# Optimization experiments

Measured on AMD Instinct MI355X. Metric: run time of the kernel, lower is better.

The kernel has to match this reference:

```python
import jax, jax.numpy as jnp
import numpy as np

EPS = 1e-6
SKIP_THR = 0.35     # AdaptiveComputeBlock skip_threshold
ENERGY_THR = 0.95   # AdaptiveRankLinear energy_threshold


def rms_norm(x, w):
    return x * jax.lax.rsqrt(jnp.mean(x * x, axis=-1, keepdims=True) + EPS) * w


def ternary_quantize(w):
    # absmean quantization: round(w/scale) clamped to {-1,0,+1}, rescaled
    s = jnp.maximum(jnp.mean(jnp.abs(w)), 1e-8)
    return jnp.clip(jnp.round(w / s), -1.0, 1.0) * s


def setup_inputs() -> dict:
    key = jax.random.key(0)
    ks = jax.random.split(key, 16)
    D, H, depth, R, N = 2048, 8192, 2, 16, 4096
    inp = {
        "x": jax.random.normal(ks[0], (N, D), jnp.float32),
        "acb_norm_w": jnp.ones((depth, D), jnp.float32),
        "router_w": jax.random.normal(ks[1], (depth, D), jnp.float32) * 0.02,
        "w1": jax.random.normal(ks[2], (depth, H, D), jnp.float32) * 0.02,
        "w2": jax.random.normal(ks[3], (depth, D, H), jnp.float32) * 0.02,
        "w3": jax.random.normal(ks[4], (depth, H, D), jnp.float32) * 0.02,
        "acb_gamma": jax.random.uniform(ks[5], (depth, D), jnp.float32) * 1e-2,
        "arl_norm_w": jnp.ones((depth, D), jnp.float32),
        "U": jax.random.normal(ks[6], (depth, D, R), jnp.float32) * 0.02,
        "S": jax.random.normal(ks[7], (depth, R), jnp.float32),
        "V": jax.random.normal(ks[8], (depth, R, D), jnp.float32) * 0.02,
        "arl_gamma": jax.random.uniform(ks[9], (depth, D), jnp.float32) * 1e-2,
        "bit_norm_w": jnp.ones((depth, D), jnp.float32),
        "w_up": jax.random.normal(ks[10], (depth, H, D), jnp.float32) * 0.02,
        "w_down": jax.random.normal(ks[11], (depth, D, H), jnp.float32) * 0.02,
        "bit_gamma": jax.random.uniform(ks[12], (depth, D), jnp.float32) * 1e-2,
    }
    return inp


def reference(x, acb_norm_w, router_w, w1, w2, w3, acb_gamma,
              arl_norm_w, U, S, V, arl_gamma,
              bit_norm_w, w_up, w_down, bit_gamma):
    depth = acb_norm_w.shape[0]
    for d in range(depth):
        # ---- AdaptiveComputeBlock (eval path: hard router mask, no gate scaling)
        xn = rms_norm(x, acb_norm_w[d])                    # [N, D]
        gates = jax.nn.sigmoid(xn @ router_w[d])           # [N]
        active = (gates > SKIP_THR)[..., None]             # [N, 1]
        h = jax.nn.silu(xn @ w1[d].T) * (xn @ w3[d].T)     # [N, H] SwiGLU
        ffn = h @ w2[d].T                                  # [N, D]
        x = x + jnp.where(active, ffn * acb_gamma[d], 0.0)

        # ---- AdaptiveRankLinear (effective-rank mask from singular energy)
        xn = rms_norm(x, arl_norm_w[d])
        s_abs = jnp.abs(S[d])
        cum = jnp.cumsum(s_abs) / jnp.maximum(jnp.sum(s_abs), 1e-8)
        # index i kept iff i < r, r = first index with cum >= threshold (plus 1)
        keep = jnp.concatenate([jnp.ones((1,), bool), cum[:-1] < ENERGY_THR])
        low = (xn @ U[d]) * (S[d] * keep)                  # [N, R]
        x = x + (low @ V[d]) * arl_gamma[d]

        # ---- BitLinear (eval path: ternary weights, fp activations)
        xn = rms_norm(x, bit_norm_w[d])
        hq = jax.nn.silu(xn @ ternary_quantize(w_up[d]).T)  # [N, H]
        x = x + (hq @ ternary_quantize(w_down[d]).T) * bit_gamma[d]
    return x
```

## Files before the change

### kernel.cpp

```cpp
#include <hip/hip_runtime.h>

#define D_DIM 2048
#define H_DIM 8192
#define NTOK  4096
#define R_DIM 16
#define DEPTH 2

typedef float f32x4 __attribute__((ext_vector_type(4)));
typedef __bf16 bf16x8 __attribute__((ext_vector_type(8)));
typedef unsigned short u16x4 __attribute__((ext_vector_type(4)));
typedef unsigned short u16x8 __attribute__((ext_vector_type(8)));
typedef int i32x4 __attribute__((ext_vector_type(4)));
typedef int i32x2 __attribute__((ext_vector_type(2)));

typedef __attribute__((address_space(1))) void void_g;
typedef __attribute__((address_space(3))) void void_l;

__device__ __forceinline__ unsigned short f2bf(float f){
  __bf16 b = (__bf16)f;
  return __builtin_bit_cast(unsigned short, b);
}
__device__ __forceinline__ float bf2f(unsigned short u){
  unsigned int x = ((unsigned int)u) << 16;
  return __builtin_bit_cast(float, x);
}

__device__ __forceinline__ float wredf(float v){
#pragma unroll
  for(int o=32;o;o>>=1) v += __shfl_xor(v,o,64);
  return v;
}
__device__ __forceinline__ float wredmax(float v){
#pragma unroll
  for(int o=32;o;o>>=1) v = fmaxf(v, __shfl_xor(v,o,64));
  return v;
}
__device__ __forceinline__ double wredd(double v){
#pragma unroll
  for(int o=32;o;o>>=1) v += __shfl_xor(v,o,64);
  return v;
}

__device__ __forceinline__ void gload_lds16(const void* g, void* l){
  __builtin_amdgcn_global_load_lds((void_g*)g, (void_l*)l, 16, 0, 0);
}

__device__ __forceinline__ int clampi(int v, int lim){
  return v > lim ? lim : (v < -lim ? -lim : v);
}
__device__ __forceinline__ int pack4q(float a, float b, float c, float d,
                                      float inv, int lim){
  int qa = clampi((int)rintf(a*inv), lim);
  int qb = clampi((int)rintf(b*inv), lim);
  int qc = clampi((int)rintf(c*inv), lim);
  int qd = clampi((int)rintf(d*inv), lim);
  return (qa&255) | ((qb&255)<<8) | ((qc&255)<<16) | ((qd&255)<<24);
}

__global__ __launch_bounds__(256) void rowpass1_i8(
    const float* __restrict__ x, const float* __restrict__ nw,
    const float* __restrict__ rw, signed char* __restrict__ xq,
    float* __restrict__ sxn, float* __restrict__ act)
{
  const int row = blockIdx.x, tid = threadIdx.x;
  const int lane = tid & 63, wid = tid >> 6;
  const float* xr = x + (size_t)row*D_DIM + tid*8;
  f32x4 v0 = *(const f32x4*)xr;
  f32x4 v1 = *(const f32x4*)(xr+4);
  float ssq = 0.0f;
#pragma unroll
  for(int j=0;j<4;++j) ssq += v0[j]*v0[j] + v1[j]*v1[j];
  __shared__ float red[4];
  float t = wredf(ssq);
  if(lane==0) red[wid] = t;
  __syncthreads();
  const float rs = rsqrtf((red[0]+red[1]+red[2]+red[3])*(1.0f/D_DIM) + 1e-6f);

  f32x4 n0 = *(const f32x4*)(nw + tid*8);
  f32x4 n1 = *(const f32x4*)(nw + tid*8 + 4);
  f32x4 r0 = *(const f32x4*)(rw + tid*8);
  f32x4 r1 = *(const f32x4*)(rw + tid*8 + 4);
  float a[8];
  float gp = 0.0f, am = 0.0f;
#pragma unroll
  for(int j=0;j<4;++j){
    a[j]   = v0[j]*rs*n0[j];
    a[4+j] = v1[j]*rs*n1[j];
    gp += a[j]*r0[j] + a[4+j]*r1[j];
    am = fmaxf(am, fmaxf(fabsf(a[j]), fabsf(a[4+j])));
  }
  float wm = wredmax(am);
  __syncthreads();
  if(lane==0) red[wid] = wm;
  __syncthreads();
  const float rowmax = fmaxf(fmaxf(red[0],red[1]), fmaxf(red[2],red[3]));
  const float guard = fmaxf(rowmax, 1e-12f);
  const float inv = 127.0f/guard;
  i32x2 q;
  q[0] = pack4q(a[0],a[1],a[2],a[3], inv, 127);
  q[1] = pack4q(a[4],a[5],a[6],a[7], inv, 127);
  *(i32x2*)(xq + (size_t)row*D_DIM + tid*8) = q;

  float gd = wredf(gp);
  __syncthreads();
  if(lane==0) red[wid] = gd;
  __syncthreads();
  if(tid==0){
    sxn[row] = guard/127.0f;
    float dot = red[0]+red[1]+red[2]+red[3];
    float g = 1.0f/(1.0f+expf(-dot));
    act[row] = (g > 0.35f) ? 1.0f : 0.0f;
  }
}

__global__ __launch_bounds__(256) void rowpass2_i8(
    float* __restrict__ x, const float* __restrict__ anw,
    const float* __restrict__ U, const float* __restrict__ Sv,
    const float* __restrict__ V, const float* __restrict__ agam,
    const float* __restrict__ bnw, signed char* __restrict__ xq,
    float* __restrict__ sxn)
{
  const int row = blockIdx.x, tid = threadIdx.x;
  const int lane = tid & 63, wid = tid >> 6;
  float* xr = x + (size_t)row*D_DIM + tid*8;
  f32x4 v0 = *(const f32x4*)xr;
  f32x4 v1 = *(const f32x4*)(xr+4);
  float ssq = 0.0f;
#pragma unroll
  for(int j=0;j<4;++j) ssq += v0[j]*v0[j] + v1[j]*v1[j];
  __shared__ float red[4];
  float t = wredf(ssq);
  if(lane==0) red[wid] = t;
  __syncthreads();
  const float rs = rsqrtf((red[0]+red[1]+red[2]+red[3])*(1.0f/D_DIM) + 1e-6f);

  f32x4 a0 = *(const f32x4*)(anw + tid*8);
  f32x4 a1 = *(const f32x4*)(anw + tid*8 + 4);
  float xn2[8];
#pragma unroll
  for(int j=0;j<4;++j){ xn2[j] = v0[j]*rs*a0[j]; xn2[4+j] = v1[j]*rs*a1[j]; }

  float pl[16];
#pragma unroll
  for(int r2=0;r2<16;++r2) pl[r2] = 0.0f;
#pragma unroll
  for(int j=0;j<8;++j){
    const int k = tid*8 + j;
    const f32x4* Up = (const f32x4*)(U + (size_t)k*R_DIM);
    f32x4 u0=Up[0], u1=Up[1], u2=Up[2], u3=Up[3];
    const float xv = xn2[j];
#pragma unroll
    for(int q=0;q<4;++q){
      pl[q]    += xv*u0[q];
      pl[4+q]  += xv*u1[q];
      pl[8+q]  += xv*u2[q];
      pl[12+q] += xv*u3[q];
    }
  }
#pragma unroll
  for(int r2=0;r2<16;++r2) pl[r2] = wredf(pl[r2]);
  __shared__ float lred[4][16];
  if(lane==0){
#pragma unroll
    for(int r2=0;r2<16;++r2) lred[wid][r2] = pl[r2];
  }
  __syncthreads();
  __shared__ float lowS[16];
  if(tid==0){
    float sa[16]; float totS = 0.0f;
#pragma unroll
    for(int r2=0;r2<16;++r2){ sa[r2] = fabsf(Sv[r2]); totS += sa[r2]; }
    totS = fmaxf(totS, 1e-8f);
    float c = 0.0f;
#pragma unroll
    for(int r2=0;r2<16;++r2){
      float lraw = lred[0][r2]+lred[1][r2]+lred[2][r2]+lred[3][r2];
      float keep = (r2==0) ? 1.0f : ((c/totS < 0.95f) ? 1.0f : 0.0f);
      c += sa[r2];
      lowS[r2] = lraw * Sv[r2] * keep;
    }
  }
  __syncthreads();

  f32x4 d0 = {0,0,0,0}, d1 = {0,0,0,0};
#pragma unroll
  for(int r2=0;r2<16;++r2){
    const float lr = lowS[r2];
    const f32x4* Vp = (const f32x4*)(V + (size_t)r2*D_DIM + tid*8);
    f32x4 q0 = Vp[0], q1 = Vp[1];
#pragma unroll
    for(int j=0;j<4;++j){ d0[j] += lr*q0[j]; d1[j] += lr*q1[j]; }
  }
  f32x4 g0 = *(const f32x4*)(agam + tid*8);
  f32x4 g1 = *(const f32x4*)(agam + tid*8 + 4);
  f32x4 xo0, xo1;
  float ssq2 = 0.0f;
#pragma unroll
  for(int j=0;j<4;++j){
    xo0[j] = v0[j] + d0[j]*g0[j];
    xo1[j] = v1[j] + d1[j]*g1[j];
    ssq2 += xo0[j]*xo0[j] + xo1[j]*xo1[j];
  }
  __syncthreads();
  float t2 = wredf(ssq2);
  if(lane==0) red[wid] = t2;
  __syncthreads();
  const float rs2 = rsqrtf((red[0]+red[1]+red[2]+red[3])*(1.0f/D_DIM) + 1e-6f);
  f32x4 b0 = *(const f32x4*)(bnw + tid*8);
  f32x4 b1 = *(const f32x4*)(bnw + tid*8 + 4);
  float a[8]; float am = 0.0f;
#pragma unroll
  for(int j=0;j<4;++j){
    a[j]   = xo0[j]*rs2*b0[j];
    a[4+j] = xo1[j]*rs2*b1[j];
    am = fmaxf(am, fmaxf(fabsf(a[j]), fabsf(a[4+j])));
  }
  *(f32x4*)xr = xo0;
  *(f32x4*)(xr+4) = xo1;

  float wm = wredmax(am);
  __syncthreads();
  if(lane==0) red[wid] = wm;
  __syncthreads();
  const float rowmax = fmaxf(fmaxf(red[0],red[1]), fmaxf(red[2],red[3]));
  const float guard = fmaxf(rowmax, 1e-12f);
  const float inv = 127.0f/guard;
  i32x2 q;
  q[0] = pack4q(a[0],a[1],a[2],a[3], inv, 127);
  q[1] = pack4q(a[4],a[5],a[6],a[7], inv, 127);
  *(i32x2*)(xq + (size_t)row*D_DIM + tid*8) = q;
  if(tid==0) sxn[row] = guard/127.0f;
}

__global__ __launch_bounds__(256) void hquant(
    const unsigned short* __restrict__ h, signed char* __restrict__ q,
    float* __restrict__ sh)
{
  const int row = blockIdx.x, tid = threadIdx.x;
  const int lane = tid & 63, wid = tid >> 6;
  const unsigned short* hr = h + (size_t)row*H_DIM + tid*32;
  float v[32]; float am = 0.0f;
#pragma unroll
  for(int c=0;c<4;++c){
    u16x8 u = *(const u16x8*)(hr + c*8);
#pragma unroll
    for(int j=0;j<8;++j){
      float f = bf2f(u[j]);
      v[c*8+j] = f;
      am = fmaxf(am, fabsf(f));
    }
  }
  __shared__ float red[4];
  float wm = wredmax(am);
  if(lane==0) red[wid] = wm;
  __syncthreads();
  const float rowmax = fmaxf(fmaxf(red[0],red[1]), fmaxf(red[2],red[3]));
  const float guard = fmaxf(rowmax, 1e-12f);
  const float inv = 127.0f/guard;
  i32x4 o0, o1;
#pragma unroll
  for(int c=0;c<4;++c){
    int p = pack4q(v[c*4],v[c*4+1],v[c*4+2],v[c*4+3], inv, 127);
    o0[c] = p;
  }
#pragma unroll
  for(int c=0;c<4;++c){
    int p = pack4q(v[16+c*4],v[16+c*4+1],v[16+c*4+2],v[16+c*4+3], inv, 127);
    o1[c] = p;
  }
  signed char* qp = q + (size_t)row*H_DIM + tid*32;
  *(i32x4*)qp = o0;
  *(i32x4*)(qp+16) = o1;
  if(tid==0) sh[row] = guard/127.0f;
}

__global__ __launch_bounds__(256) void wmax_part(const float* __restrict__ w,
                                                 float* __restrict__ part)
{
  const long long n4 = (long long)H_DIM*D_DIM/4;
  const int tid = threadIdx.x;
  const int lane = tid & 63, wid = tid >> 6;
  float m = 0.0f;
  for(long long i = (long long)blockIdx.x*256 + tid; i < n4;
      i += (long long)gridDim.x*256){
    f32x4 v = ((const f32x4*)w)[i];
    m = fmaxf(m, fmaxf(fmaxf(fabsf(v[0]),fabsf(v[1])),
                       fmaxf(fabsf(v[2]),fabsf(v[3]))));
  }
  float wm = wredmax(m);
  __shared__ float red[4];
  if(lane==0) red[wid] = wm;
  __syncthreads();
  if(tid==0) part[blockIdx.x] = fmaxf(fmaxf(red[0],red[1]),
                                      fmaxf(red[2],red[3]));
}

__global__ __launch_bounds__(256) void wmax_final(const float* __restrict__ part,
                                                  float* __restrict__ scale)
{
  const int tid = threadIdx.x;
  const int lane = tid & 63, wid = tid >> 6;
  float m = 0.0f;
  for(int i=tid;i<1024;i+=256) m = fmaxf(m, part[i]);
  m = wredmax(m);
  __shared__ float red[4];
  if(lane==0) red[wid] = m;
  __syncthreads();
  if(tid==0){
    float mm = fmaxf(fmaxf(red[0],red[1]), fmaxf(red[2],red[3]));
    scale[0] = fmaxf(mm, 1e-12f)/127.0f;
  }
}

__global__ __launch_bounds__(256) void wquant_i8(const float* __restrict__ w,
                                                 const float* __restrict__ scale,
                                                 signed char* __restrict__ q)
{
  const long long n8 = (long long)H_DIM*D_DIM/8;
  const float inv = 1.0f/scale[0];
  for(long long i = (long long)blockIdx.x*256 + threadIdx.x; i < n8;
      i += (long long)gridDim.x*256){
    f32x4 a = ((const f32x4*)w)[2*i];
    f32x4 b = ((const f32x4*)w)[2*i+1];
    i32x2 o;
    o[0] = pack4q(a[0],a[1],a[2],a[3], inv, 127);
    o[1] = pack4q(b[0],b[1],b[2],b[3], inv, 127);
    ((i32x2*)q)[i] = o;
  }
}

__global__ __launch_bounds__(256) void abs_part(const float* __restrict__ w,
                                                double* __restrict__ part)
{
  const long long n4 = (long long)H_DIM*D_DIM/4;
  const int tid = threadIdx.x;
  const int lane = tid & 63, wid = tid >> 6;
  float s = 0.0f;
  for(long long i = (long long)blockIdx.x*256 + tid; i < n4;
      i += (long long)gridDim.x*256){
    f32x4 v = ((const f32x4*)w)[i];
    s += fabsf(v[0]) + fabsf(v[1]) + fabsf(v[2]) + fabsf(v[3]);
  }
  double ds = wredd((double)s);
  __shared__ double sred[4];
  if(lane==0) sred[wid] = ds;
  __syncthreads();
  if(tid==0) part[blockIdx.x] = sred[0]+sred[1]+sred[2]+sred[3];
}

__global__ __launch_bounds__(256) void abs_final(const double* __restrict__ part,
                                                 float* __restrict__ scale)
{
  const int tid = threadIdx.x;
  const int lane = tid & 63, wid = tid >> 6;
  double s = 0.0;
  for(int i=tid;i<1024;i+=256) s += part[i];
  s = wredd(s);
  __shared__ double sred[4];
  if(lane==0) sred[wid] = s;
  __syncthreads();
  if(tid==0){
    double m = (sred[0]+sred[1]+sred[2]+sred[3]) / ((double)H_DIM*(double)D_DIM);
    scale[0] = (float)fmax(m, 1e-8);
  }
}

__global__ __launch_bounds__(256) void tquant_i8(const float* __restrict__ w,
                                                 const float* __restrict__ scale,
                                                 signed char* __restrict__ q)
{
  const long long n8 = (long long)H_DIM*D_DIM/8;
  const float inv = 1.0f/scale[0];
  for(long long i = (long long)blockIdx.x*256 + threadIdx.x; i < n8;
      i += (long long)gridDim.x*256){
    f32x4 a = ((const f32x4*)w)[2*i];
    f32x4 b = ((const f32x4*)w)[2*i+1];
    i32x2 o;
    o[0] = pack4q(a[0],a[1],a[2],a[3], inv, 1);
    o[1] = pack4q(b[0],b[1],b[2],b[3], inv, 1);
    ((i32x2*)q)[i] = o;
  }
}

template<int EPI, bool DUAL>
__global__ __launch_bounds__(256, DUAL?2:3) void gemm128q(
    const signed char* __restrict__ A,
    const signed char* __restrict__ B0,
    const signed char* __restrict__ B1,
    const int Nout, const int K,
    const float* __restrict__ sArow,
    const float* __restrict__ sW0p,
    const float* __restrict__ sW1p,
    unsigned short* __restrict__ obf,
    float* __restrict__ xacc,
    const float* __restrict__ gamma,
    const float* __restrict__ act)
{
  __shared__ __align__(16) signed char smA[128*64];
  __shared__ __align__(16) signed char smB[128*64];
  __shared__ __align__(16) signed char smB2[DUAL?(128*64):16];

  const int tid  = threadIdx.x;
  const int lane = tid & 63;
  const int wid  = tid >> 6;
  const int wr   = wid >> 1;
  const int wc   = wid & 1;
  const int frow = lane & 15;
  const int k16  = lane >> 4;

  const int nwg = (int)gridDim.x;
  const int bid = (int)blockIdx.x;
  const int swz = ((bid & 7) * (nwg >> 3)) + (bid >> 3);
  const int rowBase = (swz & 31) << 7;
  const int colBase = (swz >> 5) << 7;

  int srow[2], schk[2];
#pragma unroll
  for(int r=0;r<2;++r){
    int t = tid + (r<<8);
    srow[r] = t >> 2;
    schk[r] = (t & 3) ^ ((srow[r] >> 1) & 3);
  }

  const i32x4 izero = {0,0,0,0};
  i32x4 acc[4][4];
  i32x4 acc2[4][4];
#pragma unroll
  for(int m=0;m<4;++m)
#pragma unroll
    for(int n=0;n<4;++n){ acc[m][n] = izero; acc2[m][n] = izero; }

  for(int k0=0;k0<K;k0+=64){
#pragma unroll
    for(int r=0;r<2;++r){
      const signed char* s = A + (size_t)(rowBase+srow[r])*K + k0 + schk[r]*16;
      gload_lds16(s, &smA[((r<<8)+(wid<<6))*16]);
    }
#pragma unroll
    for(int r=0;r<2;++r){
      const signed char* s = B0 + (size_t)(colBase+srow[r])*K + k0 + schk[r]*16;
      gload_lds16(s, &smB[((r<<8)+(wid<<6))*16]);
    }
    if constexpr (DUAL){
#pragma unroll
      for(int r=0;r<2;++r){
        const signed char* s = B1 + (size_t)(colBase+srow[r])*K + k0 + schk[r]*16;
        gload_lds16(s, &smB2[((r<<8)+(wid<<6))*16]);
      }
    }
    __syncthreads();

    i32x4 af[4];
#pragma unroll
    for(int m=0;m<4;++m){
      int rr = (wr<<6)+(m<<4)+frow;
      int ch = k16 ^ ((rr>>1)&3);
      af[m] = *(const i32x4*)&smA[rr*64 + ch*16];
    }
    i32x4 bfr[4];
    i32x4 bfr2[4];
#pragma unroll
    for(int n=0;n<4;++n){
      int rr = (wc<<6)+(n<<4)+frow;
      int ch = k16 ^ ((rr>>1)&3);
      bfr[n] = *(const i32x4*)&smB[rr*64 + ch*16];
      if constexpr (DUAL) bfr2[n] = *(const i32x4*)&smB2[rr*64 + ch*16];
    }
#pragma unroll
    for(int m=0;m<4;++m)
#pragma unroll
      for(int n=0;n<4;++n){
        acc[m][n] = __builtin_amdgcn_mfma_i32_16x16x64_i8(af[m], bfr[n], acc[m][n], 0,0,0);
        if constexpr (DUAL)
          acc2[m][n] = __builtin_amdgcn_mfma_i32_16x16x64_i8(af[m], bfr2[n], acc2[m][n], 0,0,0);
      }
    __syncthreads();
  }

  const float fsW0 = sW0p[0];
  const float fsW1 = DUAL ? sW1p[0] : 0.0f;
  const int growB = rowBase + (wr<<6) + (k16<<2);
  const int gcolB = colBase + (wc<<6) + frow;
#pragma unroll
  for(int m=0;m<4;++m){
#pragma unroll
    for(int n=0;n<4;++n){
      const int grow0 = growB + (m<<4);
      const int gcol  = gcolB + (n<<4);
      i32x4 v = acc[m][n];
      if constexpr (EPI==0){
        i32x4 v2 = acc2[m][n];
#pragma unroll
        for(int j=0;j<4;++j){
          const float sa = sArow[grow0+j];
          float f1 = (float)v[j]  * sa * fsW0;
          float f3 = (float)v2[j] * sa * fsW1;
          float hv = (f1/(1.0f+expf(-f1))) * f3;
          obf[(size_t)(grow0+j)*Nout + gcol] = f2bf(hv);
        }
      } else if constexpr (EPI==1){
#pragma unroll
        for(int j=0;j<4;++j){
          const float sa = sArow[grow0+j];
          float f = (float)v[j] * sa * fsW0;
          obf[(size_t)(grow0+j)*Nout + gcol] = f2bf(f/(1.0f+expf(-f)));
        }
      } else if constexpr (EPI==2){
        const float g = gamma[gcol];
#pragma unroll
        for(int j=0;j<4;++j){
          if(act[grow0+j] != 0.0f){
            const float sa = sArow[grow0+j];
            const size_t ix = (size_t)(grow0+j)*Nout + gcol;
            xacc[ix] += (float)v[j] * sa * fsW0 * g;
          }
        }
      } else {
        const float g = gamma[gcol];
#pragma unroll
        for(int j=0;j<4;++j){
          const float sa = sArow[grow0+j];
          const size_t ix = (size_t)(grow0+j)*Nout + gcol;
          xacc[ix] += (float)v[j] * sa * fsW0 * g;
        }
      }
    }
  }
}

__global__ __launch_bounds__(256) void rowpass1(
    const float* __restrict__ x, const float* __restrict__ nw,
    const float* __restrict__ rw, unsigned short* __restrict__ xn,
    float* __restrict__ act)
{
  const int row = blockIdx.x, tid = threadIdx.x;
  const int lane = tid & 63, wid = tid >> 6;
  const float* xr = x + (size_t)row*D_DIM + tid*8;
  f32x4 v0 = *(const f32x4*)xr;
  f32x4 v1 = *(const f32x4*)(xr+4);
  float ssq = 0.0f;
#pragma unroll
  for(int j=0;j<4;++j) ssq += v0[j]*v0[j] + v1[j]*v1[j];
  __shared__ float red[4];
  float t = wredf(ssq);
  if(lane==0) red[wid] = t;
  __syncthreads();
  const float rs = rsqrtf((red[0]+red[1]+red[2]+red[3])*(1.0f/D_DIM) + 1e-6f);
  f32x4 n0 = *(const f32x4*)(nw + tid*8);
  f32x4 n1 = *(const f32x4*)(nw + tid*8 + 4);
  f32x4 r0 = *(const f32x4*)(rw + tid*8);
  f32x4 r1 = *(const f32x4*)(rw + tid*8 + 4);
  float gp = 0.0f;
  u16x4 o0, o1;
#pragma unroll
  for(int j=0;j<4;++j){
    float a = v0[j]*rs*n0[j];
    float b = v1[j]*rs*n1[j];
    gp += a*r0[j] + b*r1[j];
    o0[j] = f2bf(a);
    o1[j] = f2bf(b);
  }
  unsigned short* xp = xn + (size_t)row*D_DIM + tid*8;
  *(u16x4*)xp = o0;
  *(u16x4*)(xp+4) = o1;
  float gd = wredf(gp);
  __syncthreads();
  if(lane==0) red[wid] = gd;
  __syncthreads();
  if(tid==0){
    float dot = red[0]+red[1]+red[2]+red[3];
    float g = 1.0f/(1.0f+expf(-dot));
    act[row] = (g > 0.35f) ? 1.0f : 0.0f;
  }
}

__global__ __launch_bounds__(256) void rowpass2(
    float* __restrict__ x, const float* __restrict__ anw,
    const float* __restrict__ U, const float* __restrict__ Sv,
    const float* __restrict__ V, const float* __restrict__ agam,
    const float* __restrict__ bnw, unsigned short* __restrict__ xn3)
{
  const int row = blockIdx.x, tid = threadIdx.x;
  const int lane = tid & 63, wid = tid >> 6;
  float* xr = x + (size_t)row*D_DIM + tid*8;
  f32x4 v0 = *(const f32x4*)xr;
  f32x4 v1 = *(const f32x4*)(xr+4);
  float ssq = 0.0f;
#pragma unroll
  for(int j=0;j<4;++j) ssq += v0[j]*v0[j] + v1[j]*v1[j];
  __shared__ float red[4];
  float t = wredf(ssq);
  if(lane==0) red[wid] = t;
  __syncthreads();
  const float rs = rsqrtf((red[0]+red[1]+red[2]+red[3])*(1.0f/D_DIM) + 1e-6f);
  f32x4 a0 = *(const f32x4*)(anw + tid*8);
  f32x4 a1 = *(const f32x4*)(anw + tid*8 + 4);
  float xn2[8];
#pragma unroll
  for(int j=0;j<4;++j){ xn2[j] = v0[j]*rs*a0[j]; xn2[4+j] = v1[j]*rs*a1[j]; }
  float pl[16];
#pragma unroll
  for(int r2=0;r2<16;++r2) pl[r2] = 0.0f;
#pragma unroll
  for(int j=0;j<8;++j){
    const int k = tid*8 + j;
    const f32x4* Up = (const f32x4*)(U + (size_t)k*R_DIM);
    f32x4 u0=Up[0], u1=Up[1], u2=Up[2], u3=Up[3];
    const float xv = xn2[j];
#pragma unroll
    for(int q=0;q<4;++q){
      pl[q] += xv*u0[q]; pl[4+q] += xv*u1[q];
      pl[8+q] += xv*u2[q]; pl[12+q] += xv*u3[q];
    }
  }
#pragma unroll
  for(int r2=0;r2<16;++r2) pl[r2] = wredf(pl[r2]);
  __shared__ float lred[4][16];
  if(lane==0){
#pragma unroll
    for(int r2=0;r2<16;++r2) lred[wid][r2] = pl[r2];
  }
  __syncthreads();
  __shared__ float lowS[16];
  if(tid==0){
    float sa[16]; float totS = 0.0f;
#pragma unroll
    for(int r2=0;r2<16;++r2){ sa[r2] = fabsf(Sv[r2]); totS += sa[r2]; }
    totS = fmaxf(totS, 1e-8f);
    float c = 0.0f;
#pragma unroll
    for(int r2=0;r2<16;++r2){
      float lraw = lred[0][r2]+lred[1][r2]+lred[2][r2]+lred[3][r2];
      float keep = (r2==0) ? 1.0f : ((c/totS < 0.95f) ? 1.0f : 0.0f);
      c += sa[r2];
      lowS[r2] = lraw * Sv[r2] * keep;
    }
  }
  __syncthreads();
  f32x4 d0 = {0,0,0,0}, d1 = {0,0,0,0};
#pragma unroll
  for(int r2=0;r2<16;++r2){
    const float lr = lowS[r2];
    const f32x4* Vp = (const f32x4*)(V + (size_t)r2*D_DIM + tid*8);
    f32x4 q0 = Vp[0], q1 = Vp[1];
#pragma unroll
    for(int j=0;j<4;++j){ d0[j] += lr*q0[j]; d1[j] += lr*q1[j]; }
  }
  f32x4 g0 = *(const f32x4*)(agam + tid*8);
  f32x4 g1 = *(const f32x4*)(agam + tid*8 + 4);
  f32x4 xo0, xo1;
  float ssq2 = 0.0f;
#pragma unroll
  for(int j=0;j<4;++j){
    xo0[j] = v0[j] + d0[j]*g0[j];
    xo1[j] = v1[j] + d1[j]*g1[j];
    ssq2 += xo0[j]*xo0[j] + xo1[j]*xo1[j];
  }
  __syncthreads();
  float t2 = wredf(ssq2);
  if(lane==0) red[wid] = t2;
  __syncthreads();
  const float rs2 = rsqrtf((red[0]+red[1]+red[2]+red[3])*(1.0f/D_DIM) + 1e-6f);
  f32x4 b0 = *(const f32x4*)(bnw + tid*8);
  f32x4 b1 = *(const f32x4*)(bnw + tid*8 + 4);
  u16x4 o0, o1;
#pragma unroll
  for(int j=0;j<4;++j){
    o0[j] = f2bf(xo0[j]*rs2*b0[j]);
    o1[j] = f2bf(xo1[j]*rs2*b1[j]);
  }
  *(f32x4*)xr = xo0;
  *(f32x4*)(xr+4) = xo1;
  unsigned short* xp = xn3 + (size_t)row*D_DIM + tid*8;
  *(u16x4*)xp = o0;
  *(u16x4*)(xp+4) = o1;
}

__global__ __launch_bounds__(256) void tquant(const float* __restrict__ w,
                                              const float* __restrict__ scale,
                                              unsigned short* __restrict__ q)
{
  const long long n4 = (long long)H_DIM*D_DIM/4;
  const float s = scale[0];
  for(long long i = (long long)blockIdx.x*256 + threadIdx.x; i < n4;
      i += (long long)gridDim.x*256){
    f32x4 v = ((const f32x4*)w)[i];
    u16x4 o;
#pragma unroll
    for(int j=0;j<4;++j){
      float r = rintf(v[j]/s);
      r = fminf(1.0f, fmaxf(-1.0f, r));
      o[j] = f2bf(r*s);
    }
    ((u16x4*)q)[i] = o;
  }
}

template<int EPI, bool BBF16, bool DUAL>
__global__ __launch_bounds__(256, DUAL?2:3) void gemm128(
    const unsigned short* __restrict__ A,
    const void* __restrict__ B0v,
    const void* __restrict__ B1v,
    const int Nout, const int K,
    unsigned short* __restrict__ obf,
    float* __restrict__ xacc,
    const float* __restrict__ gamma,
    const float* __restrict__ act)
{
  __shared__ __align__(16) unsigned short smA[128*32];
  __shared__ __align__(16) unsigned short smB[128*32];
  __shared__ __align__(16) unsigned short smB2[DUAL?(128*32):8];

  const int tid  = threadIdx.x;
  const int lane = tid & 63;
  const int wid  = tid >> 6;
  const int wr   = wid >> 1;
  const int wc   = wid & 1;
  const int frow = lane & 15;
  const int k16  = lane >> 4;

  const int nwg = (int)gridDim.x;
  const int bid = (int)blockIdx.x;
  const int swz = ((bid & 7) * (nwg >> 3)) + (bid >> 3);
  const int rowBase = (swz & 31) << 7;
  const int colBase = (swz >> 5) << 7;

  int srow[2], schk[2];
#pragma unroll
  for(int r=0;r<2;++r){
    int t = tid + (r<<8);
    srow[r] = t >> 2;
    schk[r] = (t & 3) ^ ((srow[r] >> 1) & 3);
  }

  const f32x4 vzero = {0.0f,0.0f,0.0f,0.0f};
  f32x4 acc[4][4];
  f32x4 acc2[4][4];
#pragma unroll
  for(int m=0;m<4;++m)
#pragma unroll
    for(int n=0;n<4;++n){ acc[m][n] = vzero; acc2[m][n] = vzero; }

  for(int k0=0;k0<K;k0+=32){
#pragma unroll
    for(int r=0;r<2;++r){
      const unsigned short* s = A + (size_t)(rowBase+srow[r])*K + k0 + schk[r]*8;
      gload_lds16(s, &smA[((r<<8)+(wid<<6))*8]);
    }
    if constexpr (BBF16){
      const unsigned short* B0 = (const unsigned short*)B0v;
#pragma unroll
      for(int r=0;r<2;++r){
        const unsigned short* s = B0 + (size_t)(colBase+srow[r])*K + k0 + schk[r]*8;
        gload_lds16(s, &smB[((r<<8)+(wid<<6))*8]);
      }
    } else {
      const float* B0 = (const float*)B0v;
#pragma unroll
      for(int r=0;r<2;++r){
        const float* s = B0 + (size_t)(colBase+srow[r])*K + k0 + schk[r]*8;
        f32x4 f0 = *(const f32x4*)s;
        f32x4 f1 = *(const f32x4*)(s+4);
        u16x8 o;
#pragma unroll
        for(int j=0;j<4;++j){ o[j] = f2bf(f0[j]); o[4+j] = f2bf(f1[j]); }
        *(u16x8*)&smB[(size_t)(tid+(r<<8))*8] = o;
      }
      if constexpr (DUAL){
        const float* B1 = (const float*)B1v;
#pragma unroll
        for(int r=0;r<2;++r){
          const float* s = B1 + (size_t)(colBase+srow[r])*K + k0 + schk[r]*8;
          f32x4 f0 = *(const f32x4*)s;
          f32x4 f1 = *(const f32x4*)(s+4);
          u16x8 o;
#pragma unroll
          for(int j=0;j<4;++j){ o[j] = f2bf(f0[j]); o[4+j] = f2bf(f1[j]); }
          *(u16x8*)&smB2[(size_t)(tid+(r<<8))*8] = o;
        }
      }
    }
    __syncthreads();

    bf16x8 af[4];
#pragma unroll
    for(int m=0;m<4;++m){
      int rr = (wr<<6)+(m<<4)+frow;
      int ch = k16 ^ ((rr>>1)&3);
      af[m] = *(const bf16x8*)&smA[rr*32 + ch*8];
    }
    bf16x8 bfr[4];
    bf16x8 bfr2[4];
#pragma unroll
    for(int n=0;n<4;++n){
      int rr = (wc<<6)+(n<<4)+frow;
      int ch = k16 ^ ((rr>>1)&3);
      bfr[n] = *(const bf16x8*)&smB[rr*32 + ch*8];
      if constexpr (DUAL) bfr2[n] = *(const bf16x8*)&smB2[rr*32 + ch*8];
    }
#pragma unroll
    for(int m=0;m<4;++m)
#pragma unroll
      for(int n=0;n<4;++n){
        acc[m][n] = __builtin_amdgcn_mfma_f32_16x16x32_bf16(af[m], bfr[n], acc[m][n], 0,0,0);
        if constexpr (DUAL)
          acc2[m][n] = __builtin_amdgcn_mfma_f32_16x16x32_bf16(af[m], bfr2[n], acc2[m][n], 0,0,0);
      }
    __syncthreads();
  }

  const int growB = rowBase + (wr<<6) + (k16<<2);
  const int gcolB = colBase + (wc<<6) + frow;
#pragma unroll
  for(int m=0;m<4;++m){
#pragma unroll
    for(int n=0;n<4;++n){
      const int grow0 = growB + (m<<4);
      const int gcol  = gcolB + (n<<4);
      f32x4 v = acc[m][n];
      if constexpr (EPI==0){
        f32x4 v2 = acc2[m][n];
#pragma unroll
        for(int j=0;j<4;++j){
          float t1 = v[j];
          float hv = (t1/(1.0f+expf(-t1))) * v2[j];
          obf[(size_t)(grow0+j)*Nout + gcol] = f2bf(hv);
        }
      } else if constexpr (EPI==1){
#pragma unroll
        for(int j=0;j<4;++j){
          float t1 = v[j];
          obf[(size_t)(grow0+j)*Nout + gcol] = f2bf(t1/(1.0f+expf(-t1)));
        }
      } else if constexpr (EPI==2){
        const float g = gamma[gcol];
#pragma unroll
        for(int j=0;j<4;++j){
          if(act[grow0+j] != 0.0f){
            const size_t ix = (size_t)(grow0+j)*Nout + gcol;
            xacc[ix] += v[j]*g;
          }
        }
      } else {
        const float g = gamma[gcol];
#pragma unroll
        for(int j=0;j<4;++j){
          const size_t ix = (size_t)(grow0+j)*Nout + gcol;
          xacc[ix] += v[j]*g;
        }
      }
    }
  }
}

extern "C" void kernel_launch(void* const* d_in, const int* in_sizes, int n_in,
                              void* d_out, int out_size, void* d_ws, size_t ws_size,
                              hipStream_t stream)
{
  (void)in_sizes; (void)n_in; (void)out_size;
  const float* x_in  = (const float*)d_in[0];
  const float* acbnw = (const float*)d_in[1];
  const float* routw = (const float*)d_in[2];
  const float* w1    = (const float*)d_in[3];
  const float* w2    = (const float*)d_in[4];
  const float* w3    = (const float*)d_in[5];
  const float* acbg  = (const float*)d_in[6];
  const float* arlnw = (const float*)d_in[7];
  const float* U     = (const float*)d_in[8];
  const float* Sv    = (const float*)d_in[9];
  const float* V     = (const float*)d_in[10];
  const float* arlg  = (const float*)d_in[11];
  const float* bitnw = (const float*)d_in[12];
  const float* wup   = (const float*)d_in[13];
  const float* wdn   = (const float*)d_in[14];
  const float* bitg  = (const float*)d_in[15];

  float* xs = (float*)d_out;
  char* ws = (char*)d_ws;

  const bool big = (ws_size >= (size_t)185000000);

  hipMemcpyAsync(xs, x_in, (size_t)NTOK*D_DIM*sizeof(float),
                 hipMemcpyDeviceToDevice, stream);

  if (big) {
    const size_t MB = 1048576;
    unsigned short* hb   = (unsigned short*)(ws);
    signed char*    xnq  = (signed char*)(ws + 64*MB);
    signed char*    hbq  = (signed char*)(ws + 72*MB);
    signed char*    slotA= (signed char*)(ws + 104*MB);
    signed char*    slotB= (signed char*)(ws + 120*MB);
    char* tail = ws + 136*MB;
    float*  sxn   = (float*)(tail);
    float*  sh    = (float*)(tail + 16384);
    float*  act   = (float*)(tail + 32768);
    float*  fpart = (float*)(tail + 49152);
    double* dpart = (double*)(tail + 57344);
    float*  scb   = (float*)(tail + 65536);

    const int gH = 2048;
    const int gD = 512;

    for(int d=0; d<DEPTH; ++d){
      const size_t oD  = (size_t)d*D_DIM;
      const size_t oHD = (size_t)d*H_DIM*D_DIM;
      const size_t oR  = (size_t)d*R_DIM;
      const size_t oDR = (size_t)d*D_DIM*R_DIM;

      wmax_part<<<1024,256,0,stream>>>(w1+oHD, fpart);
      wmax_final<<<1,256,0,stream>>>(fpart, scb+0);
      wquant_i8<<<2048,256,0,stream>>>(w1+oHD, scb+0, slotA);
      wmax_part<<<1024,256,0,stream>>>(w3+oHD, fpart);
      wmax_final<<<1,256,0,stream>>>(fpart, scb+1);
      wquant_i8<<<2048,256,0,stream>>>(w3+oHD, scb+1, slotB);
      rowpass1_i8<<<NTOK,256,0,stream>>>(xs, acbnw+oD, routw+oD, xnq, sxn, act);
      gemm128q<0,true><<<gH,256,0,stream>>>(
          xnq, slotA, slotB, H_DIM, D_DIM, sxn, scb+0, scb+1,
          hb, nullptr, nullptr, nullptr);
      wmax_part<<<1024,256,0,stream>>>(w2+oHD, fpart);
      wmax_final<<<1,256,0,stream>>>(fpart, scb+2);
      wquant_i8<<<2048,256,0,stream>>>(w2+oHD, scb+2, slotA);
      hquant<<<NTOK,256,0,stream>>>(hb, hbq, sh);
      gemm128q<2,false><<<gD,256,0,stream>>>(
          hbq, slotA, nullptr, D_DIM, H_DIM, sh, scb+2, nullptr,
          nullptr, xs, acbg+oD, act);

      rowpass2_i8<<<NTOK,256,0,stream>>>(xs, arlnw+oD, U+oDR, Sv+oR, V+oDR,
                                         arlg+oD, bitnw+oD, xnq, sxn);

      abs_part<<<1024,256,0,stream>>>(wup+oHD, dpart);
      abs_final<<<1,256,0,stream>>>(dpart, scb+3);
      tquant_i8<<<2048,256,0,stream>>>(wup+oHD, scb+3, slotB);
      gemm128q<1,false><<<gH,256,0,stream>>>(
          xnq, slotB, nullptr, H_DIM, D_DIM, sxn, scb+3, nullptr,
          hb, nullptr, nullptr, nullptr);
      hquant<<<NTOK,256,0,stream>>>(hb, hbq, sh);
      abs_part<<<1024,256,0,stream>>>(wdn+oHD, dpart);
      abs_final<<<1,256,0,stream>>>(dpart, scb+4);
      tquant_i8<<<2048,256,0,stream>>>(wdn+oHD, scb+4, slotA);
      gemm128q<3,false><<<gD,256,0,stream>>>(
          hbq, slotA, nullptr, D_DIM, H_DIM, sh, scb+4, nullptr,
          nullptr, xs, bitg+oD, nullptr);
    }
  } else {
    unsigned short* xn = (unsigned short*)(ws);
    unsigned short* hb = (unsigned short*)(ws + 16777216);
    unsigned short* qb = (unsigned short*)(ws + 83886080);
    float*  act   = (float*)(ws + 117440512);
    double* parts = (double*)(ws + 117456896);
    float*  scal  = (float*)(ws + 117465088);

    const int gH = 2048;
    const int gD = 512;

    for(int d=0; d<DEPTH; ++d){
      const size_t oD  = (size_t)d*D_DIM;
      const size_t oHD = (size_t)d*H_DIM*D_DIM;
      const size_t oR  = (size_t)d*R_DIM;
      const size_t oDR = (size_t)d*D_DIM*R_DIM;

      rowpass1<<<NTOK,256,0,stream>>>(xs, acbnw+oD, routw+oD, xn, act);
      gemm128<0,false,true><<<gH,256,0,stream>>>(
          xn, w1+oHD, w3+oHD, H_DIM, D_DIM, hb, nullptr, nullptr, nullptr);
      gemm128<2,false,false><<<gD,256,0,stream>>>(
          hb, w2+oHD, nullptr, D_DIM, H_DIM, nullptr, xs, acbg+oD, act);

      rowpass2<<<NTOK,256,0,stream>>>(xs, arlnw+oD, U+oDR, Sv+oR, V+oDR,
                                      arlg+oD, bitnw+oD, xn);

      abs_part<<<1024,256,0,stream>>>(wup+oHD, parts);
      abs_final<<<1,256,0,stream>>>(parts, scal);
      tquant<<<2048,256,0,stream>>>(wup+oHD, scal, qb);
      gemm128<1,true,false><<<gH,256,0,stream>>>(
          xn, qb, nullptr, H_DIM, D_DIM, hb, nullptr, nullptr, nullptr);

      abs_part<<<1024,256,0,stream>>>(wdn+oHD, parts);
      abs_final<<<1,256,0,stream>>>(parts, scal);
      tquant<<<2048,256,0,stream>>>(wdn+oHD, scal, qb);
      gemm128<3,true,false><<<gD,256,0,stream>>>(
          hb, qb, nullptr, D_DIM, H_DIM, nullptr, xs, bitg+oD, nullptr);
    }
  }
}
```

Baseline: 1.675 ms.

## Compact router-active rows and skip inactive tokens in the SwiGLU FFN GEMMs

Adds a prefix-scan kernel that builds a compacted list of router-active rows. The dual W1/W3 GEMM gathers only those rows, hquant skips the tail, and the W2 GEMM scatters results back, so work for skipped tokens is not done. Weight quantization for the FFN becomes per-output-row absmax in one fused kernel, replacing the global max reduction and its two-pass launches. The GEMM K-tile also grows from 64 to 128 with a new LDS swizzle and uniform occupancy of 2. This adds a gather indirection and changes quantization granularity, and the gain depends on how many rows the router skips.

```diff
diff --git a/kernel.cpp b/kernel.cpp
--- a/kernel.cpp
+++ b/kernel.cpp
@@ -111,6 +111,39 @@
     float g = 1.0f/(1.0f+expf(-dot));
     act[row] = (g > 0.35f) ? 1.0f : 0.0f;
   }
+}
+
+__global__ __launch_bounds__(256) void buildmap(const float* __restrict__ act,
+                                                int* __restrict__ rowmap,
+                                                int* __restrict__ cntp)
+{
+  const int tid = threadIdx.x;
+  const int lane = tid & 63, wid = tid >> 6;
+  int flags[16]; int c = 0;
+#pragma unroll
+  for(int j=0;j<16;++j){
+    flags[j] = (act[tid*16+j] != 0.0f) ? 1 : 0;
+    c += flags[j];
+  }
+  int inc = c;
+#pragma unroll
+  for(int o=1;o<64;o<<=1){
+    int t = __shfl_up(inc, o, 64);
+    if(lane >= o) inc += t;
+  }
+  __shared__ int wsum[4];
+  if(lane==63) wsum[wid] = inc;
+  __syncthreads();
+  int base = inc - c;
+  for(int w=0;w<wid;++w) base += wsum[w];
+  const int total = wsum[0]+wsum[1]+wsum[2]+wsum[3];
+#pragma unroll
+  for(int j=0;j<16;++j){
+    if(flags[j]) rowmap[base++] = tid*16+j;
+  }
+  if(tid==0) cntp[0] = total;
+  __syncthreads();
+  for(int i = total + tid; i < NTOK; i += 256) rowmap[i] = 0;
 }
 
 __global__ __launch_bounds__(256) void rowpass2_i8(
@@ -234,9 +267,10 @@
 
 __global__ __launch_bounds__(256) void hquant(
     const unsigned short* __restrict__ h, signed char* __restrict__ q,
-    float* __restrict__ sh)
+    float* __restrict__ sh, const int* __restrict__ cntp)
 {
   const int row = blockIdx.x, tid = threadIdx.x;
+  if(cntp && row >= cntp[0]) return;
   const int lane = tid & 63, wid = tid >> 6;
   const unsigned short* hr = h + (size_t)row*H_DIM + tid*32;
   float v[32]; float am = 0.0f;
@@ -259,74 +293,50 @@
   const float inv = 127.0f/guard;
   i32x4 o0, o1;
 #pragma unroll
-  for(int c=0;c<4;++c){
-    int p = pack4q(v[c*4],v[c*4+1],v[c*4+2],v[c*4+3], inv, 127);
-    o0[c] = p;
-  }
-#pragma unroll
-  for(int c=0;c<4;++c){
-    int p = pack4q(v[16+c*4],v[16+c*4+1],v[16+c*4+2],v[16+c*4+3], inv, 127);
-    o1[c] = p;
-  }
+  for(int c=0;c<4;++c)
+    o0[c] = pack4q(v[c*4],v[c*4+1],v[c*4+2],v[c*4+3], inv, 127);
+#pragma unroll
+  for(int c=0;c<4;++c)
+    o1[c] = pack4q(v[16+c*4],v[16+c*4+1],v[16+c*4+2],v[16+c*4+3], inv, 127);
   signed char* qp = q + (size_t)row*H_DIM + tid*32;
   *(i32x4*)qp = o0;
   *(i32x4*)(qp+16) = o1;
   if(tid==0) sh[row] = guard/127.0f;
 }
 
-__global__ __launch_bounds__(256) void wmax_part(const float* __restrict__ w,
-                                                 float* __restrict__ part)
-{
-  const long long n4 = (long long)H_DIM*D_DIM/4;
-  const int tid = threadIdx.x;
+template<int C>
+__global__ __launch_bounds__(256) void wquant_row(const float* __restrict__ w,
+                                                  signed char* __restrict__ q,
+                                                  float* __restrict__ srow)
+{
+  constexpr int PER = C/256;
+  const int row = blockIdx.x, tid = threadIdx.x;
   const int lane = tid & 63, wid = tid >> 6;
-  float m = 0.0f;
-  for(long long i = (long long)blockIdx.x*256 + tid; i < n4;
-      i += (long long)gridDim.x*256){
-    f32x4 v = ((const f32x4*)w)[i];
-    m = fmaxf(m, fmaxf(fmaxf(fabsf(v[0]),fabsf(v[1])),
-                       fmaxf(fabsf(v[2]),fabsf(v[3]))));
-  }
-  float wm = wredmax(m);
+  const float* wr = w + (size_t)row*C + tid*PER;
+  float v[PER];
+  float am = 0.0f;
+#pragma unroll
+  for(int j=0;j<PER;j+=4){
+    f32x4 t = *(const f32x4*)(wr+j);
+#pragma unroll
+    for(int e=0;e<4;++e){ v[j+e] = t[e]; am = fmaxf(am, fabsf(t[e])); }
+  }
+  float wm = wredmax(am);
   __shared__ float red[4];
   if(lane==0) red[wid] = wm;
   __syncthreads();
-  if(tid==0) part[blockIdx.x] = fmaxf(fmaxf(red[0],red[1]),
-                                      fmaxf(red[2],red[3]));
-}
-
-__global__ __launch_bounds__(256) void wmax_final(const float* __restrict__ part,
-                                                  float* __restrict__ scale)
-{
-  const int tid = threadIdx.x;
-  const int lane = tid & 63, wid = tid >> 6;
-  float m = 0.0f;
-  for(int i=tid;i<1024;i+=256) m = fmaxf(m, part[i]);
-  m = wredmax(m);
-  __shared__ float red[4];
-  if(lane==0) red[wid] = m;
-  __syncthreads();
-  if(tid==0){
-    float mm = fmaxf(fmaxf(red[0],red[1]), fmaxf(red[2],red[3]));
-    scale[0] = fmaxf(mm, 1e-12f)/127.0f;
-  }
-}
-
-__global__ __launch_bounds__(256) void wquant_i8(const float* __restrict__ w,
-                                                 const float* __restrict__ scale,
-                                                 signed char* __restrict__ q)
-{
-  const long long n8 = (long long)H_DIM*D_DIM/8;
-  const float inv = 1.0f/scale[0];
-  for(long long i = (long long)blockIdx.x*256 + threadIdx.x; i < n8;
-      i += (long long)gridDim.x*256){
-    f32x4 a = ((const f32x4*)w)[2*i];
-    f32x4 b = ((const f32x4*)w)[2*i+1];
+  const float guard = fmaxf(fmaxf(fmaxf(red[0],red[1]),fmaxf(red[2],red[3])),
+                            1e-12f);
+  const float inv = 127.0f/guard;
+  signed char* qr = q + (size_t)row*C + tid*PER;
+#pragma unroll
+  for(int j=0;j<PER;j+=8){
     i32x2 o;
-    o[0] = pack4q(a[0],a[1],a[2],a[3], inv, 127);
-    o[1] = pack4q(b[0],b[1],b[2],b[3], inv, 127);
-    ((i32x2*)q)[i] = o;
-  }
+    o[0] = pack4q(v[j],v[j+1],v[j+2],v[j+3], inv, 127);
+    o[1] = pack4q(v[j+4],v[j+5],v[j+6],v[j+7], inv, 127);
+    *(i32x2*)(qr+j) = o;
+  }
+  if(tid==0) srow[row] = guard/127.0f;
 }
 
 __global__ __launch_bounds__(256) void abs_part(const float* __restrict__ w,
@@ -382,23 +392,33 @@
   }
 }
 
-template<int EPI, bool DUAL>
-__global__ __launch_bounds__(256, DUAL?2:3) void gemm128q(
+template<int EPI>
+__global__ __launch_bounds__(256, 2) void gemmq(
     const signed char* __restrict__ A,
     const signed char* __restrict__ B0,
     const signed char* __restrict__ B1,
     const int Nout, const int K,
     const float* __restrict__ sArow,
-    const float* __restrict__ sW0p,
-    const float* __restrict__ sW1p,
+    const float* __restrict__ sW0,
+    const float* __restrict__ sW1,
+    const int* __restrict__ rowmap,
+    const int* __restrict__ cntp,
     unsigned short* __restrict__ obf,
     float* __restrict__ xacc,
-    const float* __restrict__ gamma,
-    const float* __restrict__ act)
-{
-  __shared__ __align__(16) signed char smA[128*64];
-  __shared__ __align__(16) signed char smB[128*64];
-  __shared__ __align__(16) signed char smB2[DUAL?(128*64):16];
+    const float* __restrict__ gamma)
+{
+  constexpr bool DUAL    = (EPI==0);
+  constexpr bool GATHER  = (EPI==0);
+  constexpr bool SCATTER = (EPI==2);
+  constexpr bool CMP     = GATHER || SCATTER;
+
+  __shared__ __align__(16) signed char smA[128*128];
+  __shared__ __align__(16) signed char smB[128*128];
+  __shared__ __align__(16) signed char smB2[DUAL?(128*128):16];
+
+  int cnt = 0;
+  if constexpr (CMP) cnt = cntp[0];
+  const int padded = CMP ? ((cnt+127)&~127) : (1<<30);
 
   const int tid  = threadIdx.x;
   const int lane = tid & 63;
@@ -414,12 +434,22 @@
   const int rowBase = (swz & 31) << 7;
   const int colBase = (swz >> 5) << 7;
 
-  int srow[2], schk[2];
-#pragma unroll
-  for(int r=0;r<2;++r){
-    int t = tid + (r<<8);
-    srow[r] = t >> 2;
-    schk[r] = (t & 3) ^ ((srow[r] >> 1) & 3);
+  if constexpr (CMP){ if(rowBase >= padded) return; }
+
+  const signed char* Asrc[4];
+  const signed char* Bsrc[4];
+  const signed char* B2src[4];
+#pragma unroll
+  for(int u=0;u<4;++u){
+    int L = u*256 + tid;
+    int row = L >> 3, c = L & 7;
+    int soff = (c ^ (row & 7)) * 16;
+    int arow;
+    if constexpr (GATHER) arow = rowmap[rowBase + row];
+    else                  arow = rowBase + row;
+    Asrc[u] = A + (size_t)arow*K + soff;
+    Bsrc[u] = B0 + (size_t)(colBase + row)*K + soff;
+    if constexpr (DUAL) B2src[u] = B1 + (size_t)(colBase + row)*K + soff;
   }
 
   const i32x4 izero = {0,0,0,0};
@@ -430,55 +460,47 @@
 #pragma unroll
     for(int n=0;n<4;++n){ acc[m][n] = izero; acc2[m][n] = izero; }
 
-  for(int k0=0;k0<K;k0+=64){
-#pragma unroll
-    for(int r=0;r<2;++r){
-      const signed char* s = A + (size_t)(rowBase+srow[r])*K + k0 + schk[r]*16;
-      gload_lds16(s, &smA[((r<<8)+(wid<<6))*16]);
-    }
-#pragma unroll
-    for(int r=0;r<2;++r){
-      const signed char* s = B0 + (size_t)(colBase+srow[r])*K + k0 + schk[r]*16;
-      gload_lds16(s, &smB[((r<<8)+(wid<<6))*16]);
-    }
+  for(int k0=0;k0<K;k0+=128){
+#pragma unroll
+    for(int u=0;u<4;++u) gload_lds16(Asrc[u]+k0, &smA[u*4096 + tid*16]);
+#pragma unroll
+    for(int u=0;u<4;++u) gload_lds16(Bsrc[u]+k0, &smB[u*4096 + tid*16]);
     if constexpr (DUAL){
 #pragma unroll
-      for(int r=0;r<2;++r){
-        const signed char* s = B1 + (size_t)(colBase+srow[r])*K + k0 + schk[r]*16;
-        gload_lds16(s, &smB2[((r<<8)+(wid<<6))*16]);
+      for(int u=0;u<4;++u) gload_lds16(B2src[u]+k0, &smB2[u*4096 + tid*16]);
+    }
+    __syncthreads();
+
+#pragma unroll
+    for(int ks=0;ks<2;++ks){
+      i32x4 af[4], bfr[4], bfr2[4];
+#pragma unroll
+      for(int m=0;m<4;++m){
+        int rr = (wr<<6)+(m<<4)+frow;
+        int cc = (ks*4 + k16) ^ (rr & 7);
+        af[m] = *(const i32x4*)&smA[rr*128 + cc*16];
       }
+#pragma unroll
+      for(int n=0;n<4;++n){
+        int rr = (wc<<6)+(n<<4)+frow;
+        int cc = (ks*4 + k16) ^ (rr & 7);
+        bfr[n] = *(const i32x4*)&smB[rr*128 + cc*16];
+        if constexpr (DUAL) bfr2[n] = *(const i32x4*)&smB2[rr*128 + cc*16];
+      }
+#pragma unroll
+      for(int m=0;m<4;++m)
+#pragma unroll
+        for(int n=0;n<4;++n){
+          acc[m][n] = __builtin_amdgcn_mfma_i32_16x16x64_i8(af[m], bfr[n], acc[m][n], 0,0,0);
+          if constexpr (DUAL)
+            acc2[m][n] = __builtin_amdgcn_mfma_i32_16x16x64_i8(af[m], bfr2[n], acc2[m][n], 0,0,0);
+        }
     }
     __syncthreads();
-
-    i32x4 af[4];
-#pragma unroll
-    for(int m=0;m<4;++m){
-      int rr = (wr<<6)+(m<<4)+frow;
-      int ch = k16 ^ ((rr>>1)&3);
-      af[m] = *(const i32x4*)&smA[rr*64 + ch*16];
-    }
-    i32x4 bfr[4];
-    i32x4 bfr2[4];
-#pragma unroll
-    for(int n=0;n<4;++n){
-      int rr = (wc<<6)+(n<<4)+frow;
-      int ch = k16 ^ ((rr>>1)&3);
-      bfr[n] = *(const i32x4*)&smB[rr*64 + ch*16];
-      if constexpr (DUAL) bfr2[n] = *(const i32x4*)&smB2[rr*64 + ch*16];
-    }
-#pragma unroll
-    for(int m=0;m<4;++m)
-#pragma unroll
-      for(int n=0;n<4;++n){
-        acc[m][n] = __builtin_amdgcn_mfma_i32_16x16x64_i8(af[m], bfr[n], acc[m][n], 0,0,0);
-        if constexpr (DUAL)
-          acc2[m][n] = __builtin_amdgcn_mfma_i32_16x16x64_i8(af[m], bfr2[n], acc2[m][n], 0,0,0);
-      }
-    __syncthreads();
-  }
-
-  const float fsW0 = sW0p[0];
-  const float fsW1 = DUAL ? sW1p[0] : 0.0f;
+  }
+
+  float fsW0 = 0.0f;
+  if constexpr (EPI==1 || EPI==3) fsW0 = sW0[0];
   const int growB = rowBase + (wr<<6) + (k16<<2);
   const int gcolB = colBase + (wc<<6) + frow;
 #pragma unroll
@@ -490,13 +512,16 @@
       i32x4 v = acc[m][n];
       if constexpr (EPI==0){
         i32x4 v2 = acc2[m][n];
+        const float w0 = sW0[gcol];
+        const float w1s = sW1[gcol];
 #pragma unroll
         for(int j=0;j<4;++j){
-          const float sa = sArow[grow0+j];
-          float f1 = (float)v[j]  * sa * fsW0;
-          float f3 = (float)v2[j] * sa * fsW1;
+          const int mc = grow0 + j;
+          const float sa = sArow[rowmap[mc]];
+          float f1 = (float)v[j]  * sa * w0;
+          float f3 = (float)v2[j] * sa * w1s;
           float hv = (f1/(1.0f+expf(-f1))) * f3;
-          obf[(size_t)(grow0+j)*Nout + gcol] = f2bf(hv);
+          obf[(size_t)mc*Nout + gcol] = f2bf(hv);
         }
       } else if constexpr (EPI==1){
 #pragma unroll
@@ -506,22 +531,21 @@
           obf[(size_t)(grow0+j)*Nout + gcol] = f2bf(f/(1.0f+expf(-f)));
         }
       } else if constexpr (EPI==2){
-        const float g = gamma[gcol];
+        const float gw = sW0[gcol]*gamma[gcol];
 #pragma unroll
         for(int j=0;j<4;++j){
-          if(act[grow0+j] != 0.0f){
-            const float sa = sArow[grow0+j];
-            const size_t ix = (size_t)(grow0+j)*Nout + gcol;
-            xacc[ix] += (float)v[j] * sa * fsW0 * g;
+          const int mc = grow0 + j;
+          if(mc < cnt){
+            const float sa = sArow[mc];
+            xacc[(size_t)rowmap[mc]*Nout + gcol] += (float)v[j] * sa * gw;
           }
         }
       } else {
-        const float g = gamma[gcol];
+        const float gw = fsW0*gamma[gcol];
 #pragma unroll
         for(int j=0;j<4;++j){
           const float sa = sArow[grow0+j];
-          const size_t ix = (size_t)(grow0+j)*Nout + gcol;
-          xacc[ix] += (float)v[j] * sa * fsW0 * g;
+          xacc[(size_t)(grow0+j)*Nout + gcol] += (float)v[j] * sa * gw;
         }
       }
     }
@@ -894,9 +918,12 @@
     float*  sxn   = (float*)(tail);
     float*  sh    = (float*)(tail + 16384);
     float*  act   = (float*)(tail + 32768);
-    float*  fpart = (float*)(tail + 49152);
-    double* dpart = (double*)(tail + 57344);
-    float*  scb   = (float*)(tail + 65536);
+    double* dpart = (double*)(tail + 49152);
+    float*  scb   = (float*)(tail + 57344);
+    float*  sWA   = (float*)(tail + 65536);
+    float*  sWB   = (float*)(tail + 98304);
+    int*    rowmap= (int*)(tail + 131072);
+    int*    cntp  = (int*)(tail + 147456);
 
     const int gH = 2048;
     const int gD = 512;
@@ -907,40 +934,35 @@
       const size_t oR  = (size_t)d*R_DIM;
       const size_t oDR = (size_t)d*D_DIM*R_DIM;
 
-      wmax_part<<<1024,256,0,stream>>>(w1+oHD, fpart);
-      wmax_final<<<1,256,0,stream>>>(fpart, scb+0);
-      wquant_i8<<<2048,256,0,stream>>>(w1+oHD, scb+0, slotA);
-      wmax_part<<<1024,256,0,stream>>>(w3+oHD, fpart);
-      wmax_final<<<1,256,0,stream>>>(fpart, scb+1);
-      wquant_i8<<<2048,256,0,stream>>>(w3+oHD, scb+1, slotB);
+      wquant_row<D_DIM><<<H_DIM,256,0,stream>>>(w1+oHD, slotA, sWA);
+      wquant_row<D_DIM><<<H_DIM,256,0,stream>>>(w3+oHD, slotB, sWB);
       rowpass1_i8<<<NTOK,256,0,stream>>>(xs, acbnw+oD, routw+oD, xnq, sxn, act);
-      gemm128q<0,true><<<gH,256,0,stream>>>(
-          xnq, slotA, slotB, H_DIM, D_DIM, sxn, scb+0, scb+1,
-          hb, nullptr, nullptr, nullptr);
-      wmax_part<<<1024,256,0,stream>>>(w2+oHD, fpart);
-      wmax_final<<<1,256,0,stream>>>(fpart, scb+2);
-      wquant_i8<<<2048,256,0,stream>>>(w2+oHD, scb+2, slotA);
-      hquant<<<NTOK,256,0,stream>>>(hb, hbq, sh);
-      gemm128q<2,false><<<gD,256,0,stream>>>(
-          hbq, slotA, nullptr, D_DIM, H_DIM, sh, scb+2, nullptr,
-          nullptr, xs, acbg+oD, act);
+      buildmap<<<1,256,0,stream>>>(act, rowmap, cntp);
+      gemmq<0><<<gH,256,0,stream>>>(
+          xnq, slotA, slotB, H_DIM, D_DIM, sxn, sWA, sWB, rowmap, cntp,
+          hb, nullptr, nullptr);
+      hquant<<<NTOK,256,0,stream>>>(hb, hbq, sh, cntp);
+      wquant_row<H_DIM><<<D_DIM,256,0,stream>>>(w2+oHD, slotA, sWA);
+      gemmq<2><<<gD,256,0,stream>>>(
+          hbq, slotA, nullptr, D_DIM, H_DIM, sh, sWA, nullptr, rowmap, cntp,
+          nullptr, xs, acbg+oD);
 
       rowpass2_i8<<<NTOK,256,0,stream>>>(xs, arlnw+oD, U+oDR, Sv+oR, V+oDR,
                                          arlg+oD, bitnw+oD, xnq, sxn);
 
       abs_part<<<1024,256,0,stream>>>(wup+oHD, dpart);
-      abs_final<<<1,256,0,stream>>>(dpart, scb+3);
-      tquant_i8<<<2048,256,0,stream>>>(wup+oHD, scb+3, slotB);
-      gemm128q<1,false><<<gH,256,0,stream>>>(
-          xnq, slotB, nullptr, H_DIM, D_DIM, sxn, scb+3, nullptr,
-          hb, nullptr, nullptr, nullptr);
-      hquant<<<NTOK,256,0,stream>>>(hb, hbq, sh);
+      abs_final<<<1,256,0,stream>>>(dpart, scb+0);
+      tquant_i8<<<2048,256,0,stream>>>(wup+oHD, scb+0, slotB);
+      gemmq<1><<<gH,256,0,stream>>>(
+          xnq, slotB, nullptr, H_DIM, D_DIM, sxn, scb+0, nullptr,
+          nullptr, nullptr, hb, nullptr, nullptr);
+      hquant<<<NTOK,256,0,stream>>>(hb, hbq, sh, nullptr);
       abs_part<<<1024,256,0,stream>>>(wdn+oHD, dpart);
-      abs_final<<<1,256,0,stream>>>(dpart, scb+4);
-      tquant_i8<<<2048,256,0,stream>>>(wdn+oHD, scb+4, slotA);
-      gemm128q<3,false><<<gD,256,0,stream>>>(
-          hbq, slotA, nullptr, D_DIM, H_DIM, sh, scb+4, nullptr,
-          nullptr, xs, bitg+oD, nullptr);
+      abs_final<<<1,256,0,stream>>>(dpart, scb+1);
+      tquant_i8<<<2048,256,0,stream>>>(wdn+oHD, scb+1, slotA);
+      gemmq<3><<<gD,256,0,stream>>>(
+          hbq, slotA, nullptr, D_DIM, H_DIM, sh, scb+1, nullptr,
+          nullptr, nullptr, nullptr, xs, bitg+oD);
     }
   } else {
     unsigned short* xn = (unsigned short*)(ws);
```

New measurement: 1.420 ms. 15.2% less time.
